# Performance work log

Measured on AMD Instinct MI355X. Metric: run time of the kernel, lower is better.

The kernel has to match this reference:

```python
import jax, jax.numpy as jnp
import numpy as np

N = 100000
E = 1600000
D = 128
L = 2
NEG_SLOPE = 0.2
LN_EPS = 1e-5


def setup_inputs() -> dict:
    key = jax.random.key(0)
    ks = jax.random.split(key, 12)
    x = jax.random.normal(ks[0], (N, D), dtype=jnp.float32)
    src = jax.random.randint(ks[1], (E,), 0, N)
    dst = jax.random.randint(ks[2], (E,), 0, N)
    dst = jnp.where(src == dst, (dst + 1) % N, dst)  # no pre-existing self-loops
    edge_index = jnp.stack([src, dst]).astype(jnp.int64)
    edge_weight = jax.random.uniform(ks[3], (E,), dtype=jnp.float32)
    s = 1.0 / np.sqrt(D)
    W = jax.random.normal(ks[4], (L, D, D), dtype=jnp.float32) * s
    att_src = jax.random.normal(ks[5], (L, D), dtype=jnp.float32) * s
    att_dst = jax.random.normal(ks[6], (L, D), dtype=jnp.float32) * s
    lin_edge_w = jax.random.normal(ks[7], (L, D), dtype=jnp.float32) * s  # Linear(1, D) weight
    att_edge = jax.random.normal(ks[8], (L, D), dtype=jnp.float32) * s
    bias = jnp.zeros((L, D), dtype=jnp.float32)
    ln_gamma = jnp.ones((D,), dtype=jnp.float32)
    ln_beta = jnp.zeros((D,), dtype=jnp.float32)
    return {"x": x, "edge_index": edge_index, "edge_weight": edge_weight,
            "W": W, "att_src": att_src, "att_dst": att_dst,
            "lin_edge_w": lin_edge_w, "att_edge": att_edge, "bias": bias,
            "ln_gamma": ln_gamma, "ln_beta": ln_beta}


def _gat_layer(x, src_f, dst_f, ew_f, W, a_src, a_dst, lew, a_edge, b):
    # x: [N, D]; src_f/dst_f/ew_f already include self-loops -> [E+N]
    h = x @ W                      # [N, D]
    alpha_s = h @ a_src            # [N]
    alpha_d = h @ a_dst            # [N]
    # edge_attr = ew[:,None] * lew; (edge_attr * att_edge).sum(-1) == ew * (lew . att_edge)
    alpha_e = ew_f * jnp.dot(lew, a_edge)           # [E+N]
    logits = jax.nn.leaky_relu(alpha_s[src_f] + alpha_d[dst_f] + alpha_e, NEG_SLOPE)
    # segment softmax over incoming edges of each destination node
    m = jax.ops.segment_max(logits, dst_f, num_segments=N)   # every node has a self-loop
    p = jnp.exp(logits - m[dst_f])
    z = jax.ops.segment_sum(p, dst_f, num_segments=N)
    coef = p / z[dst_f]                                      # [E+N]
    out = jax.ops.segment_sum(h[src_f] * coef[:, None], dst_f, num_segments=N)
    return out + b


def reference(x, edge_index, edge_weight, W, att_src, att_dst, lin_edge_w, att_edge, bias, ln_gamma, ln_beta):
    src, dst = edge_index[0], edge_index[1]
    # add_self_loops with fill_value='mean': loop weight = mean of incoming edge weights
    deg = jax.ops.segment_sum(jnp.ones_like(edge_weight), dst, num_segments=N)
    loop_w = jax.ops.segment_sum(edge_weight, dst, num_segments=N) / jnp.maximum(deg, 1.0)
    ar = jnp.arange(N)
    src_f = jnp.concatenate([src, ar])
    dst_f = jnp.concatenate([dst, ar])
    ew_f = jnp.concatenate([edge_weight, loop_w])
    xx = x
    for l in range(L):
        xx = _gat_layer(xx, src_f, dst_f, ew_f, W[l], att_src[l], att_dst[l],
                        lin_edge_w[l], att_edge[l], bias[l])
        xx = jax.nn.gelu(xx, approximate=False)
    xx = x + xx
    mu = jnp.mean(xx, axis=-1, keepdims=True)
    var = jnp.mean((xx - mu) ** 2, axis=-1, keepdims=True)
    return (xx - mu) * jax.lax.rsqrt(var + LN_EPS) * ln_gamma + ln_beta
```

## Files before the change

### kernel.cpp

```cpp
#include <hip/hip_runtime.h>
#include <hip/hip_bf16.h>
#include <math.h>

#define N_NODES 100000
#define N_EDGES 1600000
#define D 128
#define NEG 0.2f
#define LN_EPS 1e-5f

#define GEMM_BLOCKS ((N_NODES + 63) / 64)
#define PLACE_BLOCKS ((N_EDGES + 1023) / 1024)
#define AGG_BLOCKS (N_NODES / 16)

typedef __attribute__((ext_vector_type(8))) short bf16x8;
typedef __attribute__((ext_vector_type(4))) float f32x4;

__device__ __forceinline__ float lrelu(float v){ return fmaxf(v, NEG * v); }
__device__ __forceinline__ float gelu_exact(float v){ return 0.5f * v * (1.0f + erff(v * 0.7071067811865476f)); }
__device__ __forceinline__ float wave_sum(float v){
#pragma unroll
  for (int o = 32; o; o >>= 1) v += __shfl_xor(v, o, 64);
  return v;
}
__device__ __forceinline__ unsigned short f2bf(float f){
  __hip_bfloat16 h = __float2bfloat16(f);
  return *(unsigned short*)&h;
}
__device__ __forceinline__ float bf_lo(unsigned u){ return __uint_as_float(u << 16); }
__device__ __forceinline__ float bf_hi(unsigned u){ return __uint_as_float(u & 0xFFFF0000u); }

__global__ __launch_bounds__(256) void k_prep(const float* __restrict__ W,
                                              unsigned short* __restrict__ wfrag,
                                              const float* __restrict__ lew,
                                              const float* __restrict__ ae,
                                              float* __restrict__ c_e){
  if (threadIdx.x < 128){
    int l = threadIdx.x >> 6;
    int lane = threadIdx.x & 63;
    const float* a = lew + l * D;
    const float* b = ae + l * D;
    float v = a[lane] * b[lane] + a[64 + lane] * b[64 + lane];
    v = wave_sum(v);
    if (lane == 0) c_e[l] = v;
  }
#pragma unroll
  for (int it = 0; it < 16; it++){
    int slot = it * 256 + threadIdx.x;
    int lane = slot & 63;
    int kc   = (slot >> 6) & 3;
    int ct   = (slot >> 8) & 7;
    int l    = (slot >> 11) & 1;
    int quad = lane >> 4, n = (lane & 15) + ct * 16;
    const float* Wl = W + l * D * D;
    bf16x8 v;
#pragma unroll
    for (int j = 0; j < 8; j++){
      int k = kc * 32 + quad * 8 + j;
      v[j] = (short)f2bf(Wl[k * D + n]);
    }
    *(bf16x8*)(wfrag + (size_t)slot * 8) = v;
  }
}

template<bool ABF>
__device__ __forceinline__ void gemm_mfma(int gb,
                                          const void* __restrict__ xin_,
                                          const unsigned short* __restrict__ wfrag_l,
                                          const float* __restrict__ att_s,
                                          const float* __restrict__ att_d,
                                          unsigned short* __restrict__ hb,
                                          float* __restrict__ alpha_s,
                                          float* __restrict__ alpha_d){
  __shared__ __align__(16) unsigned short hstage[64 * 136];
  int tid = threadIdx.x;
  int wv = tid >> 6, lane = tid & 63;
  int quad = lane >> 4, c15 = lane & 15;
  int row0 = gb * 64 + wv * 16;

  int arow = min(row0 + c15, N_NODES - 1);
  bf16x8 a[4];
  if constexpr (ABF){
    const unsigned short* xr = (const unsigned short*)xin_ + (size_t)arow * D;
#pragma unroll
    for (int kc = 0; kc < 4; kc++)
      a[kc] = *(const bf16x8*)(xr + kc * 32 + quad * 8);
  } else {
    const float* xr = (const float*)xin_ + (size_t)arow * D;
#pragma unroll
    for (int kc = 0; kc < 4; kc++){
      float4 p = *(const float4*)(xr + kc * 32 + quad * 8);
      float4 q = *(const float4*)(xr + kc * 32 + quad * 8 + 4);
      bf16x8 t;
      t[0] = (short)f2bf(p.x); t[1] = (short)f2bf(p.y);
      t[2] = (short)f2bf(p.z); t[3] = (short)f2bf(p.w);
      t[4] = (short)f2bf(q.x); t[5] = (short)f2bf(q.y);
      t[6] = (short)f2bf(q.z); t[7] = (short)f2bf(q.w);
      a[kc] = t;
    }
  }

  f32x4 acc[8];
#pragma unroll
  for (int ct = 0; ct < 8; ct++) acc[ct] = (f32x4){0.f, 0.f, 0.f, 0.f};

#pragma unroll
  for (int ct = 0; ct < 8; ct++){
#pragma unroll
    for (int kc = 0; kc < 4; kc++){
      bf16x8 b = *(const bf16x8*)(wfrag_l + ((size_t)(ct * 4 + kc) * 64 + lane) * 8);
      acc[ct] = __builtin_amdgcn_mfma_f32_16x16x32_bf16(a[kc], b, acc[ct], 0, 0, 0);
    }
  }

  float attsv[8], attdv[8];
#pragma unroll
  for (int ct = 0; ct < 8; ct++){
    attsv[ct] = att_s[ct * 16 + c15];
    attdv[ct] = att_d[ct * 16 + c15];
  }
#pragma unroll
  for (int reg = 0; reg < 4; reg++){
    float ps = 0.f, pd = 0.f;
#pragma unroll
    for (int ct = 0; ct < 8; ct++){
      ps += acc[ct][reg] * attsv[ct];
      pd += acc[ct][reg] * attdv[ct];
    }
#pragma unroll
    for (int o = 8; o; o >>= 1){
      ps += __shfl_xor(ps, o, 64);
      pd += __shfl_xor(pd, o, 64);
    }
    int row = row0 + quad * 4 + reg;
    if (c15 == reg && row < N_NODES){ alpha_s[row] = ps; alpha_d[row] = pd; }
  }

#pragma unroll
  for (int ct = 0; ct < 8; ct++)
#pragma unroll
    for (int reg = 0; reg < 4; reg++)
      hstage[(wv * 16 + quad * 4 + reg) * 136 + ct * 16 + c15] = f2bf(acc[ct][reg]);
  __syncthreads();
#pragma unroll
  for (int i = 0; i < 4; i++){
    int flat = i * 256 + tid;
    int row = flat >> 4, c = flat & 15;
    int grow = gb * 64 + row;
    if (grow < N_NODES)
      *(uint4*)(hb + (size_t)grow * D + c * 8) = *(const uint4*)(hstage + row * 136 + c * 8);
  }
}

__global__ __launch_bounds__(256, 4) void k_gemm1_place(const float* __restrict__ xin,
                                                        const unsigned short* __restrict__ wfrag,
                                                        const float* __restrict__ att_s,
                                                        const float* __restrict__ att_d,
                                                        unsigned short* __restrict__ hb,
                                                        float* __restrict__ alpha_s,
                                                        float* __restrict__ alpha_d,
                                                        const int* __restrict__ ei,
                                                        const float* __restrict__ ew,
                                                        int* __restrict__ counter, int cstride,
                                                        int2* __restrict__ csr, int cap){
  if (blockIdx.x >= PLACE_BLOCKS){
    gemm_mfma<false>(blockIdx.x - PLACE_BLOCKS, xin, wfrag, att_s, att_d, hb, alpha_s, alpha_d);
  } else {
    int pb = blockIdx.x;
    int e0 = pb * 1024 + threadIdx.x;
    int ss[4], dd[4], pp[4]; float wwv[4]; bool va[4];
#pragma unroll
    for (int i = 0; i < 4; i++){
      int e = e0 + i * 256;
      va[i] = e < N_EDGES;
      ss[i] = va[i] ? ei[e] : 0;
      dd[i] = va[i] ? ei[N_EDGES + e] : 0;
      wwv[i] = va[i] ? ew[e] : 0.f;
    }
#pragma unroll
    for (int i = 0; i < 4; i++) if (va[i]) pp[i] = atomicAdd(&counter[dd[i] * cstride], 1);
#pragma unroll
    for (int i = 0; i < 4; i++)
      if (va[i] && pp[i] < cap)
        csr[(size_t)dd[i] * cap + pp[i]] = make_int2(ss[i], __float_as_int(wwv[i]));
  }
}

__global__ __launch_bounds__(256, 4) void k_gemm_alpha(const unsigned short* __restrict__ xin,
                                                       const unsigned short* __restrict__ wfrag,
                                                       const float* __restrict__ att_s,
                                                       const float* __restrict__ att_d,
                                                       unsigned short* __restrict__ hb,
                                                       float* __restrict__ alpha_s,
                                                       float* __restrict__ alpha_d){
  gemm_mfma<true>(blockIdx.x, xin, wfrag, att_s, att_d, hb, alpha_s, alpha_d);
}

template<bool LN>
__device__ __forceinline__ void agg_core(const unsigned short* __restrict__ hb,
                                         const float* __restrict__ alpha_s,
                                         const float* __restrict__ alpha_d,
                                         const int* __restrict__ counter, int cstride,
                                         const int2* __restrict__ csr, int cap,
                                         float c,
                                         const float* __restrict__ bias_l,
                                         const float* __restrict__ xres,
                                         const float* __restrict__ gamma,
                                         const float* __restrict__ beta,
                                         int n, int cg, int qbase,
                                         float o[8]){
  int deg = counter[n * cstride];
  int dg = min(deg, cap);
  size_t rs = (size_t)n * cap;
  float ad = alpha_d[n];
  float as_n = alpha_s[n];

  uint4 u_self = *((const uint4*)(hb + (size_t)n * D) + cg);
  float4 b_lo = *(const float4*)(bias_l + cg * 8);
  float4 b_hi = *(const float4*)(bias_l + cg * 8 + 4);
  float4 xr_lo, xr_hi, g_lo, g_hi, bt_lo, bt_hi;
  if constexpr (LN){
    const float* xr = xres + (size_t)n * D + cg * 8;
    xr_lo = *(const float4*)(xr);
    xr_hi = *(const float4*)(xr + 4);
    g_lo  = *(const float4*)(gamma + cg * 8);
    g_hi  = *(const float4*)(gamma + cg * 8 + 4);
    bt_lo = *(const float4*)(beta + cg * 8);
    bt_hi = *(const float4*)(beta + cg * 8 + 4);
  }

  float z = 0.f, wsum = 0.f;
  float acc[8];
#pragma unroll
  for (int k = 0; k < 8; k++) acc[k] = 0.f;

  {
    float p = 0.f, p2 = 0.f; int s = n, s2 = n;
    if (cg < dg){
      int2 eg = csr[rs + cg];
      s = eg.x;
      float w = __int_as_float(eg.y);
      wsum += w;
      p = __expf(lrelu(alpha_s[s] + ad + c * w));
    }
    if (16 + cg < dg){
      int2 eg = csr[rs + 16 + cg];
      s2 = eg.x;
      float w = __int_as_float(eg.y);
      wsum += w;
      p2 = __expf(lrelu(alpha_s[s2] + ad + c * w));
    }
    z += p + p2;
#pragma unroll
    for (int i = 0; i < 16; i++){
      float pi = __shfl(p, qbase + i, 64);
      int   si = __shfl(s, qbase + i, 64);
      uint4 u = *((const uint4*)(hb + (size_t)si * D) + cg);
      acc[0] += pi * bf_lo(u.x); acc[1] += pi * bf_hi(u.x);
      acc[2] += pi * bf_lo(u.y); acc[3] += pi * bf_hi(u.y);
      acc[4] += pi * bf_lo(u.z); acc[5] += pi * bf_hi(u.z);
      acc[6] += pi * bf_lo(u.w); acc[7] += pi * bf_hi(u.w);
    }
#pragma unroll
    for (int i = 0; i < 16; i++){
      float pi = __shfl(p2, qbase + i, 64);
      int   si = __shfl(s2, qbase + i, 64);
      uint4 u = *((const uint4*)(hb + (size_t)si * D) + cg);
      acc[0] += pi * bf_lo(u.x); acc[1] += pi * bf_hi(u.x);
      acc[2] += pi * bf_lo(u.y); acc[3] += pi * bf_hi(u.y);
      acc[4] += pi * bf_lo(u.z); acc[5] += pi * bf_hi(u.z);
      acc[6] += pi * bf_lo(u.w); acc[7] += pi * bf_hi(u.w);
    }
  }
  for (int base = 32; base < dg; base += 16){
    int j = base + cg;
    float p = 0.f; int s = n;
    if (j < dg){
      int2 eg = csr[rs + j];
      s = eg.x;
      float w = __int_as_float(eg.y);
      wsum += w;
      p = __expf(lrelu(alpha_s[s] + ad + c * w));
    }
    z += p;
#pragma unroll
    for (int i = 0; i < 16; i++){
      float pi = __shfl(p, qbase + i, 64);
      int   si = __shfl(s, qbase + i, 64);
      uint4 u = *((const uint4*)(hb + (size_t)si * D) + cg);
      acc[0] += pi * bf_lo(u.x); acc[1] += pi * bf_hi(u.x);
      acc[2] += pi * bf_lo(u.y); acc[3] += pi * bf_hi(u.y);
      acc[4] += pi * bf_lo(u.z); acc[5] += pi * bf_hi(u.z);
      acc[6] += pi * bf_lo(u.w); acc[7] += pi * bf_hi(u.w);
    }
  }
#pragma unroll
  for (int ofs = 8; ofs; ofs >>= 1){
    z += __shfl_xor(z, ofs, 64);
    wsum += __shfl_xor(wsum, ofs, 64);
  }

  float lw = wsum / fmaxf((float)deg, 1.0f);
  float ps = __expf(lrelu(as_n + ad + c * lw));
  z += ps;
  acc[0] += ps * bf_lo(u_self.x); acc[1] += ps * bf_hi(u_self.x);
  acc[2] += ps * bf_lo(u_self.y); acc[3] += ps * bf_hi(u_self.y);
  acc[4] += ps * bf_lo(u_self.z); acc[5] += ps * bf_hi(u_self.z);
  acc[6] += ps * bf_lo(u_self.w); acc[7] += ps * bf_hi(u_self.w);

  float inv = 1.0f / z;
  float bv[8] = {b_lo.x, b_lo.y, b_lo.z, b_lo.w, b_hi.x, b_hi.y, b_hi.z, b_hi.w};
#pragma unroll
  for (int k = 0; k < 8; k++) o[k] = gelu_exact(acc[k] * inv + bv[k]);

  if constexpr (LN){
    float xrv[8] = {xr_lo.x, xr_lo.y, xr_lo.z, xr_lo.w, xr_hi.x, xr_hi.y, xr_hi.z, xr_hi.w};
    float s1 = 0.f;
#pragma unroll
    for (int k = 0; k < 8; k++){ o[k] += xrv[k]; s1 += o[k]; }
#pragma unroll
    for (int ofs = 8; ofs; ofs >>= 1) s1 += __shfl_xor(s1, ofs, 64);
    float mu = s1 * (1.0f / D);
    float s2 = 0.f;
#pragma unroll
    for (int k = 0; k < 8; k++){ o[k] -= mu; s2 += o[k] * o[k]; }
#pragma unroll
    for (int ofs = 8; ofs; ofs >>= 1) s2 += __shfl_xor(s2, ofs, 64);
    float rinv = rsqrtf(s2 * (1.0f / D) + LN_EPS);
    float gv[8] = {g_lo.x, g_lo.y, g_lo.z, g_lo.w, g_hi.x, g_hi.y, g_hi.z, g_hi.w};
    float btv[8] = {bt_lo.x, bt_lo.y, bt_lo.z, bt_lo.w, bt_hi.x, bt_hi.y, bt_hi.z, bt_hi.w};
#pragma unroll
    for (int k = 0; k < 8; k++) o[k] = o[k] * rinv * gv[k] + btv[k];
  }
}

__global__ __launch_bounds__(256) void k_agg1_fused(const unsigned short* __restrict__ hb,
                                                    const float* __restrict__ alpha_s,
                                                    const float* __restrict__ alpha_d,
                                                    const int* __restrict__ counter, int cstride,
                                                    const int2* __restrict__ csr, int cap,
                                                    const float* __restrict__ c_e,
                                                    const float* __restrict__ bias,
                                                    const unsigned short* __restrict__ wfrag2,
                                                    const float* __restrict__ att_s2,
                                                    const float* __restrict__ att_d2,
                                                    unsigned short* __restrict__ hb2,
                                                    float* __restrict__ alpha2_s,
                                                    float* __restrict__ alpha2_d){
  __shared__ __align__(16) unsigned short astage[16 * 136];
  __shared__ float apart_s[16], apart_d[16];
  int tid = threadIdx.x;
  int lane = tid & 63;
  int cg = lane & 15;
  int qbase = lane & 48;
  int n = blockIdx.x * 16 + (tid >> 4);

  float o[8];
  agg_core<false>(hb, alpha_s, alpha_d, counter, cstride, csr, cap, c_e[0],
                  bias, nullptr, nullptr, nullptr, n, cg, qbase, o);

  unsigned short ob[8];
#pragma unroll
  for (int k = 0; k < 8; k++) ob[k] = f2bf(o[k]);
  *(uint4*)(astage + (tid >> 4) * 136 + cg * 8) = *(const uint4*)ob;
  if (tid < 16){ apart_s[tid] = 0.f; apart_d[tid] = 0.f; }
  __syncthreads();

  int wv = tid >> 6;
  int quad = lane >> 4, c15 = lane & 15;
  bf16x8 a[4];
#pragma unroll
  for (int kc = 0; kc < 4; kc++)
    a[kc] = *(const bf16x8*)(astage + c15 * 136 + kc * 32 + quad * 8);

  f32x4 acc2[2];
  float attsv[2], attdv[2];
#pragma unroll
  for (int t = 0; t < 2; t++){
    int ct = wv * 2 + t;
    acc2[t] = (f32x4){0.f, 0.f, 0.f, 0.f};
#pragma unroll
    for (int kc = 0; kc < 4; kc++){
      bf16x8 b = *(const bf16x8*)(wfrag2 + ((size_t)(ct * 4 + kc) * 64 + lane) * 8);
      acc2[t] = __builtin_amdgcn_mfma_f32_16x16x32_bf16(a[kc], b, acc2[t], 0, 0, 0);
    }
    attsv[t] = att_s2[ct * 16 + c15];
    attdv[t] = att_d2[ct * 16 + c15];
  }

#pragma unroll
  for (int reg = 0; reg < 4; reg++){
    float ps = acc2[0][reg] * attsv[0] + acc2[1][reg] * attsv[1];
    float pd = acc2[0][reg] * attdv[0] + acc2[1][reg] * attdv[1];
#pragma unroll
    for (int ofs = 8; ofs; ofs >>= 1){
      ps += __shfl_xor(ps, ofs, 64);
      pd += __shfl_xor(pd, ofs, 64);
    }
    if (c15 == reg){
      atomicAdd(&apart_s[quad * 4 + reg], ps);
      atomicAdd(&apart_d[quad * 4 + reg], pd);
    }
  }
  __syncthreads();

#pragma unroll
  for (int t = 0; t < 2; t++){
    int ct = wv * 2 + t;
#pragma unroll
    for (int reg = 0; reg < 4; reg++)
      astage[(quad * 4 + reg) * 136 + ct * 16 + c15] = f2bf(acc2[t][reg]);
  }
  __syncthreads();

  {
    int row = tid >> 4, ccol = tid & 15;
    int grow = blockIdx.x * 16 + row;
    *(uint4*)(hb2 + (size_t)grow * D + ccol * 8) = *(const uint4*)(astage + row * 136 + ccol * 8);
  }
  if (tid < 16){
    int grow = blockIdx.x * 16 + tid;
    alpha2_s[grow] = apart_s[tid];
    alpha2_d[grow] = apart_d[tid];
  }
}

__global__ __launch_bounds__(256) void k_agg1_plain(const unsigned short* __restrict__ hb,
                                                    const float* __restrict__ alpha_s,
                                                    const float* __restrict__ alpha_d,
                                                    const int* __restrict__ counter, int cstride,
                                                    const int2* __restrict__ csr, int cap,
                                                    const float* __restrict__ c_e,
                                                    const float* __restrict__ bias,
                                                    unsigned short* __restrict__ outp_bf){
  int tid = threadIdx.x;
  int lane = tid & 63;
  int cg = lane & 15;
  int qbase = lane & 48;
  int n = blockIdx.x * 16 + (tid >> 4);
  float o[8];
  agg_core<false>(hb, alpha_s, alpha_d, counter, cstride, csr, cap, c_e[0],
                  bias, nullptr, nullptr, nullptr, n, cg, qbase, o);
  unsigned short ob[8];
#pragma unroll
  for (int k = 0; k < 8; k++) ob[k] = f2bf(o[k]);
  *(uint4*)(outp_bf + (size_t)n * D + cg * 8) = *(const uint4*)ob;
}

__global__ __launch_bounds__(256) void k_agg2(const unsigned short* __restrict__ hb,
                                              const float* __restrict__ alpha_s,
                                              const float* __restrict__ alpha_d,
                                              const int* __restrict__ counter, int cstride,
                                              const int2* __restrict__ csr, int cap,
                                              const float* __restrict__ c_e,
                                              const float* __restrict__ bias,
                                              const float* __restrict__ xres,
                                              const float* __restrict__ gamma,
                                              const float* __restrict__ beta,
                                              float* __restrict__ outp){
  int tid = threadIdx.x;
  int lane = tid & 63;
  int cg = lane & 15;
  int qbase = lane & 48;
  int n = blockIdx.x * 16 + (tid >> 4);
  float o[8];
  agg_core<true>(hb, alpha_s, alpha_d, counter, cstride, csr, cap, c_e[1],
                 bias + D, xres, gamma, beta, n, cg, qbase, o);
  float* orow = outp + (size_t)n * D + cg * 8;
  *(float4*)(orow)     = make_float4(o[0], o[1], o[2], o[3]);
  *(float4*)(orow + 4) = make_float4(o[4], o[5], o[6], o[7]);
}

extern "C" void kernel_launch(void* const* d_in, const int* in_sizes, int n_in,
                              void* d_out, int out_size, void* d_ws, size_t ws_size,
                              hipStream_t stream) {
  const float* x     = (const float*)d_in[0];
  const int*   ei    = (const int*)d_in[1];
  const float* ew    = (const float*)d_in[2];
  const float* W     = (const float*)d_in[3];
  const float* att_s = (const float*)d_in[4];
  const float* att_d = (const float*)d_in[5];
  const float* lew   = (const float*)d_in[6];
  const float* ae    = (const float*)d_in[7];
  const float* bias  = (const float*)d_in[8];
  const float* gamma = (const float*)d_in[9];
  const float* beta  = (const float*)d_in[10];
  float* out = (float*)d_out;

  const int N = N_NODES;

  size_t hbB = (size_t)N * D * 2;
  size_t fixP = ((size_t)(16 * N) + 4 * N + 16) * 4 + 65536;
  size_t fix1 = ((size_t)N + 4 * N + 16) * 4 + 65536;
  int cstride; bool fused; int cap;
  if      (ws_size >= fixP + (size_t)N * 64 * 8 + 2 * hbB){ cstride = 16; fused = true;  cap = 64; }
  else if (ws_size >= fixP + (size_t)N * 48 * 8 + 2 * hbB){ cstride = 16; fused = true;  cap = 48; }
  else if (ws_size >= fix1 + (size_t)N * 64 * 8 + 2 * hbB){ cstride = 1;  fused = true;  cap = 64; }
  else if (ws_size >= fix1 + (size_t)N * 64 * 8 + hbB)    { cstride = 1;  fused = false; cap = 64; }
  else                                                     { cstride = 1;  fused = false; cap = 48; }

  int*   counter  = (int*)d_ws;
  float* alpha_s  = (float*)(counter + (size_t)N * cstride);
  float* alpha_d  = alpha_s + N;
  float* alpha2_s = alpha_d + N;
  float* alpha2_d = alpha2_s + N;
  float* c_e      = alpha2_d + N;
  unsigned short* wfrag = (unsigned short*)(c_e + 16);
  int2*  csr      = (int2*)(wfrag + 32768);
  unsigned short* hb  = (unsigned short*)(csr + (size_t)N * cap);
  unsigned short* hb2 = hb + (size_t)N * D;

  hipMemsetAsync(counter, 0, (size_t)N * cstride * sizeof(int), stream);
  k_prep<<<1, 256, 0, stream>>>(W, wfrag, lew, ae, c_e);

  k_gemm1_place<<<GEMM_BLOCKS + PLACE_BLOCKS, 256, 0, stream>>>(
      x, wfrag, att_s, att_d, hb, alpha_s, alpha_d, ei, ew, counter, cstride, csr, cap);

  if (fused){
    k_agg1_fused<<<AGG_BLOCKS, 256, 0, stream>>>(
        hb, alpha_s, alpha_d, counter, cstride, csr, cap, c_e, bias,
        wfrag + 16384, att_s + D, att_d + D, hb2, alpha2_s, alpha2_d);
    k_agg2<<<AGG_BLOCKS, 256, 0, stream>>>(
        hb2, alpha2_s, alpha2_d, counter, cstride, csr, cap, c_e, bias, x, gamma, beta, out);
  } else {
    unsigned short* h1b = (unsigned short*)d_out;
    k_agg1_plain<<<AGG_BLOCKS, 256, 0, stream>>>(
        hb, alpha_s, alpha_d, counter, cstride, csr, cap, c_e, bias, h1b);
    k_gemm_alpha<<<GEMM_BLOCKS, 256, 0, stream>>>(
        h1b, wfrag + 16384, att_s + D, att_d + D, hb, alpha_s, alpha_d);
    k_agg2<<<AGG_BLOCKS, 256, 0, stream>>>(
        hb, alpha_s, alpha_d, counter, cstride, csr, cap, c_e, bias, x, gamma, beta, out);
  }
}
```

Before: 429.1 us.

## Aggregate each node with 32 lanes and 8 nodes per block

The GAT aggregation kernels now map each destination node to 32 lanes handling 4 features each, instead of 16 lanes handling 8, so each block covers 8 nodes and the grid doubles. Neighbour edges are processed 32 at a time per wave with 8-byte gathers, and launch bounds ask for 8 blocks per CU. The fused layer-2 GEMM tile now carries only 8 valid rows in a 16-row MFMA tile. This spreads each node's variable-degree edge work over more lanes and raises occupancy, at the cost of narrower loads and half-idle MFMA rows in the fused kernel.

Measured after the change: 498.5 us. 1.16x slower.

```diff
diff --git a/kernel.cpp b/kernel.cpp
--- a/kernel.cpp
+++ b/kernel.cpp
@@ -10,7 +10,7 @@
 
 #define GEMM_BLOCKS ((N_NODES + 63) / 64)
 #define PLACE_BLOCKS ((N_EDGES + 1023) / 1024)
-#define AGG_BLOCKS (N_NODES / 16)
+#define AGG_BLOCKS (N_NODES / 8)
 
 typedef __attribute__((ext_vector_type(8))) short bf16x8;
 typedef __attribute__((ext_vector_type(4))) float f32x4;
@@ -196,83 +196,49 @@
 }
 
 template<bool LN>
-__device__ __forceinline__ void agg_core(const unsigned short* __restrict__ hb,
-                                         const float* __restrict__ alpha_s,
-                                         const float* __restrict__ alpha_d,
-                                         const int* __restrict__ counter, int cstride,
-                                         const int2* __restrict__ csr, int cap,
-                                         float c,
-                                         const float* __restrict__ bias_l,
-                                         const float* __restrict__ xres,
-                                         const float* __restrict__ gamma,
-                                         const float* __restrict__ beta,
-                                         int n, int cg, int qbase,
-                                         float o[8]){
+__device__ __forceinline__ void agg_core32(const unsigned short* __restrict__ hb,
+                                           const float* __restrict__ alpha_s,
+                                           const float* __restrict__ alpha_d,
+                                           const int* __restrict__ counter, int cstride,
+                                           const int2* __restrict__ csr, int cap,
+                                           float c,
+                                           const float* __restrict__ bias_l,
+                                           const float* __restrict__ xres,
+                                           const float* __restrict__ gamma,
+                                           const float* __restrict__ beta,
+                                           int n, int gl, int qb,
+                                           float o[4]){
   int deg = counter[n * cstride];
   int dg = min(deg, cap);
   size_t rs = (size_t)n * cap;
   float ad = alpha_d[n];
   float as_n = alpha_s[n];
-
-  uint4 u_self = *((const uint4*)(hb + (size_t)n * D) + cg);
-  float4 b_lo = *(const float4*)(bias_l + cg * 8);
-  float4 b_hi = *(const float4*)(bias_l + cg * 8 + 4);
-  float4 xr_lo, xr_hi, g_lo, g_hi, bt_lo, bt_hi;
-  if constexpr (LN){
-    const float* xr = xres + (size_t)n * D + cg * 8;
-    xr_lo = *(const float4*)(xr);
-    xr_hi = *(const float4*)(xr + 4);
-    g_lo  = *(const float4*)(gamma + cg * 8);
-    g_hi  = *(const float4*)(gamma + cg * 8 + 4);
-    bt_lo = *(const float4*)(beta + cg * 8);
-    bt_hi = *(const float4*)(beta + cg * 8 + 4);
-  }
+  uint2 u_self = *((const uint2*)(hb + (size_t)n * D) + gl);
 
   float z = 0.f, wsum = 0.f;
-  float acc[8];
-#pragma unroll
-  for (int k = 0; k < 8; k++) acc[k] = 0.f;
+  float acc[4] = {0.f, 0.f, 0.f, 0.f};
 
   {
-    float p = 0.f, p2 = 0.f; int s = n, s2 = n;
-    if (cg < dg){
-      int2 eg = csr[rs + cg];
+    float p = 0.f; int s = n;
+    if (gl < dg){
+      int2 eg = csr[rs + gl];
       s = eg.x;
       float w = __int_as_float(eg.y);
       wsum += w;
       p = __expf(lrelu(alpha_s[s] + ad + c * w));
     }
-    if (16 + cg < dg){
-      int2 eg = csr[rs + 16 + cg];
-      s2 = eg.x;
-      float w = __int_as_float(eg.y);
-      wsum += w;
-      p2 = __expf(lrelu(alpha_s[s2] + ad + c * w));
-    }
-    z += p + p2;
-#pragma unroll
-    for (int i = 0; i < 16; i++){
-      float pi = __shfl(p, qbase + i, 64);
-      int   si = __shfl(s, qbase + i, 64);
-      uint4 u = *((const uint4*)(hb + (size_t)si * D) + cg);
+    z += p;
+#pragma unroll
+    for (int i = 0; i < 32; i++){
+      float pi = __shfl(p, qb + i, 64);
+      int   si = __shfl(s, qb + i, 64);
+      uint2 u = *((const uint2*)(hb + (size_t)si * D) + gl);
       acc[0] += pi * bf_lo(u.x); acc[1] += pi * bf_hi(u.x);
       acc[2] += pi * bf_lo(u.y); acc[3] += pi * bf_hi(u.y);
-      acc[4] += pi * bf_lo(u.z); acc[5] += pi * bf_hi(u.z);
-      acc[6] += pi * bf_lo(u.w); acc[7] += pi * bf_hi(u.w);
-    }
-#pragma unroll
-    for (int i = 0; i < 16; i++){
-      float pi = __shfl(p2, qbase + i, 64);
-      int   si = __shfl(s2, qbase + i, 64);
-      uint4 u = *((const uint4*)(hb + (size_t)si * D) + cg);
-      acc[0] += pi * bf_lo(u.x); acc[1] += pi * bf_hi(u.x);
-      acc[2] += pi * bf_lo(u.y); acc[3] += pi * bf_hi(u.y);
-      acc[4] += pi * bf_lo(u.z); acc[5] += pi * bf_hi(u.z);
-      acc[6] += pi * bf_lo(u.w); acc[7] += pi * bf_hi(u.w);
-    }
-  }
-  for (int base = 32; base < dg; base += 16){
-    int j = base + cg;
+    }
+  }
+  for (int base = 32; base < dg; base += 32){
+    int j = base + gl;
     float p = 0.f; int s = n;
     if (j < dg){
       int2 eg = csr[rs + j];
@@ -283,18 +249,16 @@
     }
     z += p;
 #pragma unroll
-    for (int i = 0; i < 16; i++){
-      float pi = __shfl(p, qbase + i, 64);
-      int   si = __shfl(s, qbase + i, 64);
-      uint4 u = *((const uint4*)(hb + (size_t)si * D) + cg);
+    for (int i = 0; i < 32; i++){
+      float pi = __shfl(p, qb + i, 64);
+      int   si = __shfl(s, qb + i, 64);
+      uint2 u = *((const uint2*)(hb + (size_t)si * D) + gl);
       acc[0] += pi * bf_lo(u.x); acc[1] += pi * bf_hi(u.x);
       acc[2] += pi * bf_lo(u.y); acc[3] += pi * bf_hi(u.y);
-      acc[4] += pi * bf_lo(u.z); acc[5] += pi * bf_hi(u.z);
-      acc[6] += pi * bf_lo(u.w); acc[7] += pi * bf_hi(u.w);
-    }
-  }
-#pragma unroll
-  for (int ofs = 8; ofs; ofs >>= 1){
+    }
+  }
+#pragma unroll
+  for (int ofs = 16; ofs; ofs >>= 1){
     z += __shfl_xor(z, ofs, 64);
     wsum += __shfl_xor(wsum, ofs, 64);
   }
@@ -304,73 +268,75 @@
   z += ps;
   acc[0] += ps * bf_lo(u_self.x); acc[1] += ps * bf_hi(u_self.x);
   acc[2] += ps * bf_lo(u_self.y); acc[3] += ps * bf_hi(u_self.y);
-  acc[4] += ps * bf_lo(u_self.z); acc[5] += ps * bf_hi(u_self.z);
-  acc[6] += ps * bf_lo(u_self.w); acc[7] += ps * bf_hi(u_self.w);
 
   float inv = 1.0f / z;
-  float bv[8] = {b_lo.x, b_lo.y, b_lo.z, b_lo.w, b_hi.x, b_hi.y, b_hi.z, b_hi.w};
-#pragma unroll
-  for (int k = 0; k < 8; k++) o[k] = gelu_exact(acc[k] * inv + bv[k]);
+  float4 b = *(const float4*)(bias_l + gl * 4);
+  o[0] = gelu_exact(acc[0] * inv + b.x);
+  o[1] = gelu_exact(acc[1] * inv + b.y);
+  o[2] = gelu_exact(acc[2] * inv + b.z);
+  o[3] = gelu_exact(acc[3] * inv + b.w);
 
   if constexpr (LN){
-    float xrv[8] = {xr_lo.x, xr_lo.y, xr_lo.z, xr_lo.w, xr_hi.x, xr_hi.y, xr_hi.z, xr_hi.w};
-    float s1 = 0.f;
-#pragma unroll
-    for (int k = 0; k < 8; k++){ o[k] += xrv[k]; s1 += o[k]; }
-#pragma unroll
-    for (int ofs = 8; ofs; ofs >>= 1) s1 += __shfl_xor(s1, ofs, 64);
+    float4 xr = *(const float4*)(xres + (size_t)n * D + gl * 4);
+    o[0] += xr.x; o[1] += xr.y; o[2] += xr.z; o[3] += xr.w;
+    float s1 = o[0] + o[1] + o[2] + o[3];
+#pragma unroll
+    for (int ofs = 16; ofs; ofs >>= 1) s1 += __shfl_xor(s1, ofs, 64);
     float mu = s1 * (1.0f / D);
     float s2 = 0.f;
 #pragma unroll
-    for (int k = 0; k < 8; k++){ o[k] -= mu; s2 += o[k] * o[k]; }
-#pragma unroll
-    for (int ofs = 8; ofs; ofs >>= 1) s2 += __shfl_xor(s2, ofs, 64);
+    for (int k = 0; k < 4; k++){ o[k] -= mu; s2 += o[k] * o[k]; }
+#pragma unroll
+    for (int ofs = 16; ofs; ofs >>= 1) s2 += __shfl_xor(s2, ofs, 64);
     float rinv = rsqrtf(s2 * (1.0f / D) + LN_EPS);
-    float gv[8] = {g_lo.x, g_lo.y, g_lo.z, g_lo.w, g_hi.x, g_hi.y, g_hi.z, g_hi.w};
-    float btv[8] = {bt_lo.x, bt_lo.y, bt_lo.z, bt_lo.w, bt_hi.x, bt_hi.y, bt_hi.z, bt_hi.w};
-#pragma unroll
-    for (int k = 0; k < 8; k++) o[k] = o[k] * rinv * gv[k] + btv[k];
-  }
-}
-
-__global__ __launch_bounds__(256) void k_agg1_fused(const unsigned short* __restrict__ hb,
-                                                    const float* __restrict__ alpha_s,
-                                                    const float* __restrict__ alpha_d,
-                                                    const int* __restrict__ counter, int cstride,
-                                                    const int2* __restrict__ csr, int cap,
-                                                    const float* __restrict__ c_e,
-                                                    const float* __restrict__ bias,
-                                                    const unsigned short* __restrict__ wfrag2,
-                                                    const float* __restrict__ att_s2,
-                                                    const float* __restrict__ att_d2,
-                                                    unsigned short* __restrict__ hb2,
-                                                    float* __restrict__ alpha2_s,
-                                                    float* __restrict__ alpha2_d){
+    float4 g  = *(const float4*)(gamma + gl * 4);
+    float4 bt = *(const float4*)(beta + gl * 4);
+    o[0] = o[0] * rinv * g.x + bt.x;
+    o[1] = o[1] * rinv * g.y + bt.y;
+    o[2] = o[2] * rinv * g.z + bt.z;
+    o[3] = o[3] * rinv * g.w + bt.w;
+  }
+}
+
+__global__ __launch_bounds__(256, 8) void k_agg1_fused(const unsigned short* __restrict__ hb,
+                                                       const float* __restrict__ alpha_s,
+                                                       const float* __restrict__ alpha_d,
+                                                       const int* __restrict__ counter, int cstride,
+                                                       const int2* __restrict__ csr, int cap,
+                                                       const float* __restrict__ c_e,
+                                                       const float* __restrict__ bias,
+                                                       const unsigned short* __restrict__ wfrag2,
+                                                       const float* __restrict__ att_s2,
+                                                       const float* __restrict__ att_d2,
+                                                       unsigned short* __restrict__ hb2,
+                                                       float* __restrict__ alpha2_s,
+                                                       float* __restrict__ alpha2_d){
   __shared__ __align__(16) unsigned short astage[16 * 136];
-  __shared__ float apart_s[16], apart_d[16];
+  __shared__ float apart_s[8], apart_d[8];
   int tid = threadIdx.x;
   int lane = tid & 63;
-  int cg = lane & 15;
-  int qbase = lane & 48;
-  int n = blockIdx.x * 16 + (tid >> 4);
-
-  float o[8];
-  agg_core<false>(hb, alpha_s, alpha_d, counter, cstride, csr, cap, c_e[0],
-                  bias, nullptr, nullptr, nullptr, n, cg, qbase, o);
-
-  unsigned short ob[8];
-#pragma unroll
-  for (int k = 0; k < 8; k++) ob[k] = f2bf(o[k]);
-  *(uint4*)(astage + (tid >> 4) * 136 + cg * 8) = *(const uint4*)ob;
-  if (tid < 16){ apart_s[tid] = 0.f; apart_d[tid] = 0.f; }
+  int gl = lane & 31;
+  int qb = lane & 32;
+  int n = blockIdx.x * 8 + (tid >> 5);
+
+  float o[4];
+  agg_core32<false>(hb, alpha_s, alpha_d, counter, cstride, csr, cap, c_e[0],
+                    bias, nullptr, nullptr, nullptr, n, gl, qb, o);
+
+  unsigned short ob[4];
+#pragma unroll
+  for (int k = 0; k < 4; k++) ob[k] = f2bf(o[k]);
+  *((uint2*)(astage + (tid >> 5) * 136) + gl) = *(const uint2*)ob;
+  if (tid < 8){ apart_s[tid] = 0.f; apart_d[tid] = 0.f; }
   __syncthreads();
 
   int wv = tid >> 6;
   int quad = lane >> 4, c15 = lane & 15;
+  int arow = c15 & 7;
   bf16x8 a[4];
 #pragma unroll
   for (int kc = 0; kc < 4; kc++)
-    a[kc] = *(const bf16x8*)(astage + c15 * 136 + kc * 32 + quad * 8);
+    a[kc] = *(const bf16x8*)(astage + arow * 136 + kc * 32 + quad * 8);
 
   f32x4 acc2[2];
   float attsv[2], attdv[2];
@@ -396,9 +362,10 @@
       ps += __shfl_xor(ps, ofs, 64);
       pd += __shfl_xor(pd, ofs, 64);
     }
-    if (c15 == reg){
-      atomicAdd(&apart_s[quad * 4 + reg], ps);
-      atomicAdd(&apart_d[quad * 4 + reg], pd);
+    int row = quad * 4 + reg;
+    if (c15 == reg && row < 8){
+      atomicAdd(&apart_s[row], ps);
+      atomicAdd(&apart_d[row], pd);
     }
   }
   __syncthreads();
@@ -413,61 +380,59 @@
   __syncthreads();
 
   {
-    int row = tid >> 4, ccol = tid & 15;
-    int grow = blockIdx.x * 16 + row;
-    *(uint4*)(hb2 + (size_t)grow * D + ccol * 8) = *(const uint4*)(astage + row * 136 + ccol * 8);
-  }
-  if (tid < 16){
-    int grow = blockIdx.x * 16 + tid;
+    int row = tid >> 5, gcol = tid & 31;
+    int grow = blockIdx.x * 8 + row;
+    *((uint2*)(hb2 + (size_t)grow * D) + gcol) = *((const uint2*)(astage + row * 136) + gcol);
+  }
+  if (tid < 8){
+    int grow = blockIdx.x * 8 + tid;
     alpha2_s[grow] = apart_s[tid];
     alpha2_d[grow] = apart_d[tid];
   }
 }
 
-__global__ __launch_bounds__(256) void k_agg1_plain(const unsigned short* __restrict__ hb,
-                                                    const float* __restrict__ alpha_s,
-                                                    const float* __restrict__ alpha_d,
-                                                    const int* __restrict__ counter, int cstride,
-                                                    const int2* __restrict__ csr, int cap,
-                                                    const float* __restrict__ c_e,
-                                                    const float* __restrict__ bias,
-                                                    unsigned short* __restrict__ outp_bf){
+__global__ __launch_bounds__(256, 8) void k_agg1_plain(const unsigned short* __restrict__ hb,
+                                                       const float* __restrict__ alpha_s,
+                                                       const float* __restrict__ alpha_d,
+                                                       const int* __restrict__ counter, int cstride,
+                                                       const int2* __restrict__ csr, int cap,
+                                                       const float* __restrict__ c_e,
+                                                       const float* __restrict__ bias,
+                                                       unsigned short* __restrict__ outp_bf){
   int tid = threadIdx.x;
   int lane = tid & 63;
-  int cg = lane & 15;
-  int qbase = lane & 48;
-  int n = blockIdx.x * 16 + (tid >> 4);
-  float o[8];
-  agg_core<false>(hb, alpha_s, alpha_d, counter, cstride, csr, cap, c_e[0],
-                  bias, nullptr, nullptr, nullptr, n, cg, qbase, o);
-  unsigned short ob[8];
-#pragma unroll
-  for (int k = 0; k < 8; k++) ob[k] = f2bf(o[k]);
-  *(uint4*)(outp_bf + (size_t)n * D + cg * 8) = *(const uint4*)ob;
-}
-
-__global__ __launch_bounds__(256) void k_agg2(const unsigned short* __restrict__ hb,
-                                              const float* __restrict__ alpha_s,
-                                              const float* __restrict__ alpha_d,
-                                              const int* __restrict__ counter, int cstride,
-                                              const int2* __restrict__ csr, int cap,
-                                              const float* __restrict__ c_e,
-                                              const float* __restrict__ bias,
-                                              const float* __restrict__ xres,
-                                              const float* __restrict__ gamma,
-                                              const float* __restrict__ beta,
-                                              float* __restrict__ outp){
+  int gl = lane & 31;
+  int qb = lane & 32;
+  int n = blockIdx.x * 8 + (tid >> 5);
+  float o[4];
+  agg_core32<false>(hb, alpha_s, alpha_d, counter, cstride, csr, cap, c_e[0],
+                    bias, nullptr, nullptr, nullptr, n, gl, qb, o);
+  unsigned short ob[4];
+#pragma unroll
+  for (int k = 0; k < 4; k++) ob[k] = f2bf(o[k]);
+  *((uint2*)(outp_bf + (size_t)n * D) + gl) = *(const uint2*)ob;
+}
+
+__global__ __launch_bounds__(256, 8) void k_agg2(const unsigned short* __restrict__ hb,
+                                                 const float* __restrict__ alpha_s,
+                                                 const float* __restrict__ alpha_d,
+                                                 const int* __restrict__ counter, int cstride,
+                                                 const int2* __restrict__ csr, int cap,
+                                                 const float* __restrict__ c_e,
+                                                 const float* __restrict__ bias,
+                                                 const float* __restrict__ xres,
+                                                 const float* __restrict__ gamma,
+                                                 const float* __restrict__ beta,
+                                                 float* __restrict__ outp){
   int tid = threadIdx.x;
   int lane = tid & 63;
-  int cg = lane & 15;
-  int qbase = lane & 48;
-  int n = blockIdx.x * 16 + (tid >> 4);
-  float o[8];
-  agg_core<true>(hb, alpha_s, alpha_d, counter, cstride, csr, cap, c_e[1],
-                 bias + D, xres, gamma, beta, n, cg, qbase, o);
-  float* orow = outp + (size_t)n * D + cg * 8;
-  *(float4*)(orow)     = make_float4(o[0], o[1], o[2], o[3]);
-  *(float4*)(orow + 4) = make_float4(o[4], o[5], o[6], o[7]);
+  int gl = lane & 31;
+  int qb = lane & 32;
+  int n = blockIdx.x * 8 + (tid >> 5);
+  float o[4];
+  agg_core32<true>(hb, alpha_s, alpha_d, counter, cstride, csr, cap, c_e[1],
+                   bias + D, xres, gamma, beta, n, gl, qb, o);
+  *(float4*)(outp + (size_t)n * D + gl * 4) = make_float4(o[0], o[1], o[2], o[3]);
 }
 
 extern "C" void kernel_launch(void* const* d_in, const int* in_sizes, int n_in,
```
